# Kernel optimization log

Hardware: AMD Instinct MI355X
Metric: run time of the kernel (lower is better)

Reference implementation:

```python
import jax, jax.numpy as jnp
import numpy as np
import math


def _rope(x, cos, sin):
    # x: [B, S, h, hd]; cos/sin: [S, hd//2]
    B, S, h, hd = x.shape
    xr = x.reshape(B, S, h, hd // 2, 2)
    x_re, x_im = xr[..., 0], xr[..., 1]
    c = cos[None, :, None, :]
    s = sin[None, :, None, :]
    out_re = x_re * c - x_im * s
    out_im = x_re * s + x_im * c
    return jnp.stack([out_re, out_im], axis=-1).reshape(B, S, h, hd)


def setup_inputs() -> dict:
    key = jax.random.key(0)
    ks = jax.random.split(key, 8)
    B, S, D = 2, 2048, 2048
    H, G = 16, 4
    hd = D // H  # 128
    q = jax.random.normal(ks[0], (B, S, D), dtype=jnp.float32)
    k = jax.random.normal(ks[1], (B, S, D), dtype=jnp.float32)
    v = jax.random.normal(ks[2], (B, S, D), dtype=jnp.float32)
    # causal mask, matching typical usage (mask==0 -> -inf)
    mask = jnp.broadcast_to(jnp.tril(jnp.ones((S, S), dtype=jnp.int32)), (B, S, S))
    # RoPE freqs: thetas = base**(-2*arange(0,hd,2)/hd), freq = outer(m, thetas)
    exp = -2.0 * jnp.arange(0, hd, 2, dtype=jnp.float32) / hd
    thetas = jnp.power(10000.0, exp)
    m = jnp.arange(S, dtype=jnp.float32)
    freq = jnp.outer(m, thetas)  # [S, hd//2]
    freq_cos = jnp.cos(freq)
    freq_sin = jnp.sin(freq)
    sc = 0.02
    W_q = jax.random.normal(ks[3], (D, D), dtype=jnp.float32) * sc
    W_k = jax.random.normal(ks[4], (D, D // G), dtype=jnp.float32) * sc
    W_v = jax.random.normal(ks[5], (D, D // G), dtype=jnp.float32) * sc
    W_o = jax.random.normal(ks[6], (D, D), dtype=jnp.float32) * sc
    return {"q": q, "k": k, "v": v, "mask": mask, "freq_cos": freq_cos,
            "freq_sin": freq_sin, "W_q": W_q, "W_k": W_k, "W_v": W_v,
            "W_o": W_o, "heads": 16, "group_size": 4}


def reference(q, k, v, mask, freq_cos, freq_sin, W_q, W_k, W_v, W_o, heads, group_size):
    B, S, D = q.shape
    H = heads
    Hkv = H // group_size
    hd = D // H
    qp = (q @ W_q).reshape(B, S, H, hd)
    kp = (k @ W_k).reshape(B, S, Hkv, hd)
    vp = (v @ W_v).reshape(B, S, Hkv, hd)
    qp = _rope(qp, freq_cos, freq_sin)
    kp = _rope(kp, freq_cos, freq_sin)
    # repeat_kv: each kv head repeated group_size times (group index inner)
    kp = jnp.repeat(kp, group_size, axis=2)  # [B,S,H,hd]
    vp = jnp.repeat(vp, group_size, axis=2)
    qh = qp.transpose(0, 2, 1, 3)  # [B,H,S,hd]
    kh = kp.transpose(0, 2, 1, 3)
    vh = vp.transpose(0, 2, 1, 3)
    scores = jnp.einsum('bhqd,bhkd->bhqk', qh, kh) / math.sqrt(hd)
    scores = jnp.where(mask[:, None, :, :] == 0, jnp.float32(-1e9), scores)
    attn = jax.nn.softmax(scores, axis=-1)
    out = jnp.einsum('bhqk,bhkd->bhqd', attn, vh)  # [B,H,S,hd]
    out = out.transpose(0, 2, 1, 3).reshape(B, S, D)
    return out @ W_o
```

## Files before the change

kernel.cpp:

```cpp
#include <hip/hip_runtime.h>

typedef __bf16 bf16;
typedef __attribute__((ext_vector_type(8))) __bf16 bf16x8;
typedef __attribute__((ext_vector_type(4))) __bf16 bf16x4;
typedef __attribute__((ext_vector_type(4))) float f32x4;

#define MFMA16(a, b, c) __builtin_amdgcn_mfma_f32_16x16x32_bf16((a), (b), (c), 0, 0, 0)

typedef __attribute__((address_space(1))) const void* gas_t;
typedef __attribute__((address_space(3))) void* las_t;
#define GLOAD_LDS16(g, l) \
    __builtin_amdgcn_global_load_lds((gas_t)(g), (las_t)(l), 16, 0, 0)

__device__ __forceinline__ unsigned pack2(float a, float b) {
    unsigned short ua = __builtin_bit_cast(unsigned short, (bf16)a);
    unsigned short ub = __builtin_bit_cast(unsigned short, (bf16)b);
    return ((unsigned)ub << 16) | (unsigned)ua;
}

__global__ void transpose_cvt4(const float* __restrict__ Wq,
                               const float* __restrict__ Wo,
                               const float* __restrict__ Wk,
                               const float* __restrict__ Wv,
                               bf16* __restrict__ WqT, bf16* __restrict__ WoT,
                               bf16* __restrict__ WkT, bf16* __restrict__ WvT) {
    __shared__ bf16 tile[32][33];
    int z = blockIdx.z;
    const float* W = (z == 0) ? Wq : (z == 1) ? Wo : (z == 2) ? Wk : Wv;
    bf16* Wt = (z == 0) ? WqT : (z == 1) ? WoT : (z == 2) ? WkT : WvT;
    int N = (z < 2) ? 2048 : 512;
    const int K = 2048;
    int n0 = blockIdx.x * 32;
    if (n0 >= N) return;
    int k0 = blockIdx.y * 32;
    int tx = threadIdx.x, ty = threadIdx.y;
#pragma unroll
    for (int j = 0; j < 4; ++j)
        tile[ty + j * 8][tx] = (bf16)W[(size_t)(k0 + ty + j * 8) * N + n0 + tx];
    __syncthreads();
#pragma unroll
    for (int j = 0; j < 4; ++j)
        Wt[(size_t)(n0 + ty + j * 8) * K + k0 + tx] = tile[tx][ty + j * 8];
}

template <bool A_F32, bool DO_ROPE, int OUT_MODE>
__global__ __launch_bounds__(256) void gemm_bt(
    const void* __restrict__ Ain, const bf16* __restrict__ Bt,
    void* __restrict__ Cout, const float* __restrict__ cosb,
    const float* __restrict__ sinb, float scale, int Nn, int Kk) {
    __shared__ bf16 As[128 * 64];
    __shared__ bf16 Bs[128 * 64];
    int tid = threadIdx.x;
    int lane = tid & 63, wid = tid >> 6;
    int lr = lane & 15, lg = lane >> 4;
    int m0 = blockIdx.y * 128, n0 = blockIdx.x * 128;
    int wr = wid >> 1, wc = wid & 1;

    int srow = lane >> 3;
    int scol = ((lane & 7) ^ srow) << 3;
    const bf16* Bbase = Bt + (size_t)(n0 + wid * 32 + srow) * Kk + scol;
    const bf16* Abase_h =
        A_F32 ? nullptr
              : (const bf16*)Ain + (size_t)(m0 + wid * 32 + srow) * Kk + scol;

    int fragAr = wr * 64 + lr;
    int fragBr = wc * 64 + lr;
    int swz = lr & 7;

    f32x4 acc[4][4] = {};

    const int nk = Kk >> 6;
    for (int kt = 0; kt < nk; ++kt) {
        int k0 = kt << 6;
        if constexpr (A_F32) {
            const float* A = (const float*)Ain;
#pragma unroll
            for (int i = 0; i < 8; ++i) {
                int slot = tid + i * 256;
                int row = slot >> 4, c4 = (slot & 15) << 2;
                f32x4 v = *reinterpret_cast<const f32x4*>(
                    A + (size_t)(m0 + row) * Kk + k0 + c4);
                bf16x4 h;
                h[0] = (bf16)v[0]; h[1] = (bf16)v[1];
                h[2] = (bf16)v[2]; h[3] = (bf16)v[3];
                int blk = (c4 >> 3) ^ (row & 7);
                *reinterpret_cast<bf16x4*>(
                    &As[row * 64 + (blk << 3) + (c4 & 7)]) = h;
            }
        } else {
#pragma unroll
            for (int i = 0; i < 4; ++i)
                GLOAD_LDS16(Abase_h + (size_t)(i * 8) * Kk + k0,
                            &As[(wid * 4 + i) * 512]);
        }
#pragma unroll
        for (int i = 0; i < 4; ++i)
            GLOAD_LDS16(Bbase + (size_t)(i * 8) * Kk + k0,
                        &Bs[(wid * 4 + i) * 512]);
        __syncthreads();
#pragma unroll
        for (int kk = 0; kk < 2; ++kk) {
            int colOff = ((((kk << 2) | lg) ^ swz) << 3);
            bf16x8 af[4], bfr[4];
#pragma unroll
            for (int mi = 0; mi < 4; ++mi)
                af[mi] = *reinterpret_cast<const bf16x8*>(
                    &As[(fragAr + mi * 16) * 64 + colOff]);
#pragma unroll
            for (int ni = 0; ni < 4; ++ni)
                bfr[ni] = *reinterpret_cast<const bf16x8*>(
                    &Bs[(fragBr + ni * 16) * 64 + colOff]);
#pragma unroll
            for (int mi = 0; mi < 4; ++mi)
#pragma unroll
                for (int ni = 0; ni < 4; ++ni)
                    acc[mi][ni] = MFMA16(af[mi], bfr[ni], acc[mi][ni]);
        }
        __syncthreads();
    }

    int m_base = m0 + wr * 64, n_base = n0 + wc * 64;
#pragma unroll
    for (int mi = 0; mi < 4; ++mi) {
#pragma unroll
        for (int ni = 0; ni < 4; ++ni) {
            f32x4 v = acc[mi][ni];
            int gn = n_base + ni * 16 + lr;
            if constexpr (DO_ROPE) {
                int d = gn & 127, p = d >> 1;
                bool ev = ((d & 1) == 0);
#pragma unroll
                for (int r = 0; r < 4; ++r) {
                    int gm = m_base + mi * 16 + lg * 4 + r;
                    int s = gm & 2047;
                    float cc = cosb[s * 64 + p];
                    float ss = sinb[s * 64 + p];
                    float oth = __shfl_xor(v[r], 1);
                    v[r] = (ev ? (v[r] * cc - oth * ss)
                               : (oth * ss + v[r] * cc)) * scale;
                }
            }
            if constexpr (OUT_MODE == 0) {
                bf16* C = (bf16*)Cout;
#pragma unroll
                for (int r = 0; r < 4; ++r)
                    C[(size_t)(m_base + mi * 16 + lg * 4 + r) * Nn + gn] =
                        (bf16)v[r];
            } else {
                float* C = (float*)Cout;
#pragma unroll
                for (int r = 0; r < 4; ++r)
                    C[(size_t)(m_base + mi * 16 + lg * 4 + r) * Nn + gn] = v[r];
            }
        }
    }
}

__global__ __launch_bounds__(256) void gemm_kv(
    const float* __restrict__ kin, const float* __restrict__ vin,
    const bf16* __restrict__ WkT, const bf16* __restrict__ WvT,
    bf16* __restrict__ Kt, bf16* __restrict__ Vt,
    const float* __restrict__ cosb, const float* __restrict__ sinb) {
    const int Nn = 512, Kk = 2048;
    __shared__ bf16 As[128 * 64];
    __shared__ bf16 Bs[128 * 64];
    bool isK = (blockIdx.z == 0);
    const float* A = isK ? kin : vin;
    const bf16* Bt = isK ? WkT : WvT;

    int tid = threadIdx.x;
    int lane = tid & 63, wid = tid >> 6;
    int lr = lane & 15, lg = lane >> 4;
    int m0 = blockIdx.y * 128, n0 = blockIdx.x * 128;
    int wr = wid >> 1, wc = wid & 1;

    int srow = lane >> 3;
    int scol = ((lane & 7) ^ srow) << 3;
    const bf16* Bbase = Bt + (size_t)(n0 + wid * 32 + srow) * Kk + scol;

    int fragAr = wr * 64 + lr;
    int fragBr = wc * 64 + lr;
    int swz = lr & 7;

    f32x4 acc[4][4] = {};

    for (int kt = 0; kt < 32; ++kt) {
        int k0 = kt << 6;
#pragma unroll
        for (int i = 0; i < 8; ++i) {
            int slot = tid + i * 256;
            int row = slot >> 4, c4 = (slot & 15) << 2;
            f32x4 v = *reinterpret_cast<const f32x4*>(
                A + (size_t)(m0 + row) * Kk + k0 + c4);
            bf16x4 h;
            h[0] = (bf16)v[0]; h[1] = (bf16)v[1];
            h[2] = (bf16)v[2]; h[3] = (bf16)v[3];
            int blk = (c4 >> 3) ^ (row & 7);
            *reinterpret_cast<bf16x4*>(&As[row * 64 + (blk << 3) + (c4 & 7)]) = h;
        }
#pragma unroll
        for (int i = 0; i < 4; ++i)
            GLOAD_LDS16(Bbase + (size_t)(i * 8) * Kk + k0,
                        &Bs[(wid * 4 + i) * 512]);
        __syncthreads();
#pragma unroll
        for (int kk = 0; kk < 2; ++kk) {
            int colOff = ((((kk << 2) | lg) ^ swz) << 3);
            bf16x8 af[4], bfr[4];
#pragma unroll
            for (int mi = 0; mi < 4; ++mi)
                af[mi] = *reinterpret_cast<const bf16x8*>(
                    &As[(fragAr + mi * 16) * 64 + colOff]);
#pragma unroll
            for (int ni = 0; ni < 4; ++ni)
                bfr[ni] = *reinterpret_cast<const bf16x8*>(
                    &Bs[(fragBr + ni * 16) * 64 + colOff]);
#pragma unroll
            for (int mi = 0; mi < 4; ++mi)
#pragma unroll
                for (int ni = 0; ni < 4; ++ni)
                    acc[mi][ni] = MFMA16(af[mi], bfr[ni], acc[mi][ni]);
        }
        __syncthreads();
    }

    int m_base = m0 + wr * 64, n_base = n0 + wc * 64;
#pragma unroll
    for (int mi = 0; mi < 4; ++mi) {
#pragma unroll
        for (int ni = 0; ni < 4; ++ni) {
            f32x4 v = acc[mi][ni];
            int gn = n_base + ni * 16 + lr;
            int hkv = gn >> 7, d = gn & 127;
            if (isK) {
                int p = d >> 1;
                bool ev = ((d & 1) == 0);
#pragma unroll
                for (int r = 0; r < 4; ++r) {
                    int gm = m_base + mi * 16 + lg * 4 + r;
                    int s = gm & 2047;
                    float cc = cosb[s * 64 + p];
                    float ss = sinb[s * 64 + p];
                    float oth = __shfl_xor(v[r], 1);
                    float rv = ev ? (v[r] * cc - oth * ss) : (oth * ss + v[r] * cc);
                    int bb = gm >> 11;
                    Kt[((size_t)(bb * 4 + hkv) * 2048 + s) * 128 + d] = (bf16)rv;
                }
            } else {
                int gm0 = m_base + mi * 16 + lg * 4;
                int bb = gm0 >> 11, s = gm0 & 2047;
                bf16x4 hh;
#pragma unroll
                for (int r = 0; r < 4; ++r) hh[r] = (bf16)v[r];
                *reinterpret_cast<bf16x4*>(
                    Vt + ((size_t)(bb * 4 + hkv) * 128 + d) * 2048 + s) = hh;
            }
        }
    }
}

__global__ __launch_bounds__(256) void attn_kernel(
    const bf16* __restrict__ Qp, const bf16* __restrict__ Kt,
    const bf16* __restrict__ Vt, bf16* __restrict__ Ao) {
    const int S = 2048, H = 16, HKV = 4, HD = 128;
    __shared__ bf16 Klds[64][136];
    __shared__ bf16 Vlds[128][72];

    int tid = threadIdx.x, lane = tid & 63, wid = tid >> 6;
    int lr = lane & 15, lg = lane >> 4;
    int h = blockIdx.x, b = blockIdx.y;
    int qt = (int)(gridDim.z - 1) - (int)blockIdx.z;
    int hkv = h >> 2;
    int q0 = qt * 64 + wid * 16;
    int qrow = q0 + lr;

    const bf16* Kbase = Kt + (size_t)(b * HKV + hkv) * S * HD;
    const bf16* Vbase = Vt + (size_t)(b * HKV + hkv) * HD * S;

    bf16x8 qf[4];
    {
        const bf16* qb = Qp + ((size_t)(b * S + qrow) * H + h) * HD;
#pragma unroll
        for (int ks = 0; ks < 4; ++ks)
            qf[ks] = *reinterpret_cast<const bf16x8*>(qb + ks * 32 + lg * 8);
    }

    f32x4 O[8] = {};
    float m_run = -3e38f, l_run = 0.f;
    int src0 = ((lane >> 4) & 1) * 32 + lr;
    int src1 = src0 + 16;
    bool h1 = (lg >> 1) != 0;

    for (int kb = 0; kb <= qt; ++kb) {
        int s0 = kb * 64;
        bf16x8 kreg[4], vreg[4];
#pragma unroll
        for (int i = 0; i < 4; ++i) {
            int slot = tid + i * 256;
            int krow = slot >> 4, kc = (slot & 15) << 3;
            kreg[i] = *reinterpret_cast<const bf16x8*>(
                Kbase + (size_t)(s0 + krow) * HD + kc);
            int vrow = slot >> 3, vc = (slot & 7) << 3;
            vreg[i] = *reinterpret_cast<const bf16x8*>(
                Vbase + (size_t)vrow * S + s0 + vc);
        }
#pragma unroll
        for (int i = 0; i < 4; ++i) {
            int slot = tid + i * 256;
            int krow = slot >> 4, kc = (slot & 15) << 3;
            *reinterpret_cast<bf16x8*>(&Klds[krow][kc]) = kreg[i];
            int vrow = slot >> 3, vc = (slot & 7) << 3;
            *reinterpret_cast<bf16x8*>(&Vlds[vrow][vc]) = vreg[i];
        }
        __syncthreads();

        float p[4][4];
#pragma unroll
        for (int nt = 0; nt < 4; ++nt) {
            f32x4 sc = {};
#pragma unroll
            for (int ks = 0; ks < 4; ++ks) {
                bf16x8 kf = *reinterpret_cast<const bf16x8*>(
                    &Klds[nt * 16 + lr][ks * 32 + lg * 8]);
                sc = MFMA16(kf, qf[ks], sc);
            }
            if (kb == qt) {
                int sa = s0 + nt * 16 + lg * 4;
#pragma unroll
                for (int r = 0; r < 4; ++r)
                    p[nt][r] = (sa + r <= qrow) ? sc[r] : -1e30f;
            } else {
#pragma unroll
                for (int r = 0; r < 4; ++r) p[nt][r] = sc[r];
            }
        }
        float mx = p[0][0];
#pragma unroll
        for (int nt = 0; nt < 4; ++nt)
#pragma unroll
            for (int r = 0; r < 4; ++r) mx = fmaxf(mx, p[nt][r]);
        mx = fmaxf(mx, __shfl_xor(mx, 16));
        mx = fmaxf(mx, __shfl_xor(mx, 32));
        float mnew = fmaxf(m_run, mx);
        float al = __expf(m_run - mnew);
        m_run = mnew;
        float rs = 0.f;
#pragma unroll
        for (int nt = 0; nt < 4; ++nt)
#pragma unroll
            for (int r = 0; r < 4; ++r) {
                p[nt][r] = __expf(p[nt][r] - mnew);
                rs += p[nt][r];
            }
        rs += __shfl_xor(rs, 16);
        rs += __shfl_xor(rs, 32);
        l_run = l_run * al + rs;

        unsigned pk00 = pack2(p[0][0], p[0][1]), pk01 = pack2(p[0][2], p[0][3]);
        unsigned pk10 = pack2(p[1][0], p[1][1]), pk11 = pack2(p[1][2], p[1][3]);
        unsigned pk20 = pack2(p[2][0], p[2][1]), pk21 = pack2(p[2][2], p[2][3]);
        unsigned pk30 = pack2(p[3][0], p[3][1]), pk31 = pack2(p[3][2], p[3][3]);
        unsigned e00 = __shfl(pk00, src0), e01 = __shfl(pk01, src0);
        unsigned e10 = __shfl(pk10, src0), e11 = __shfl(pk11, src0);
        unsigned e20 = __shfl(pk20, src0), e21 = __shfl(pk21, src0);
        unsigned e30 = __shfl(pk30, src0), e31 = __shfl(pk31, src0);
        unsigned o00 = __shfl(pk00, src1), o01 = __shfl(pk01, src1);
        unsigned o10 = __shfl(pk10, src1), o11 = __shfl(pk11, src1);
        unsigned o20 = __shfl(pk20, src1), o21 = __shfl(pk21, src1);
        unsigned o30 = __shfl(pk30, src1), o31 = __shfl(pk31, src1);
        union U { unsigned u[4]; bf16x8 v; } P0, P1;
        P0.u[0] = h1 ? e10 : e00;
        P0.u[1] = h1 ? e11 : e01;
        P0.u[2] = h1 ? o10 : o00;
        P0.u[3] = h1 ? o11 : o01;
        P1.u[0] = h1 ? e30 : e20;
        P1.u[1] = h1 ? e31 : e21;
        P1.u[2] = h1 ? o30 : o20;
        P1.u[3] = h1 ? o31 : o21;

#pragma unroll
        for (int d2 = 0; d2 < 8; ++d2)
#pragma unroll
            for (int r = 0; r < 4; ++r) O[d2][r] *= al;
#pragma unroll
        for (int d2 = 0; d2 < 8; ++d2) {
            bf16x8 vf0 =
                *reinterpret_cast<const bf16x8*>(&Vlds[d2 * 16 + lr][lg * 8]);
            bf16x8 vf1 = *reinterpret_cast<const bf16x8*>(
                &Vlds[d2 * 16 + lr][32 + lg * 8]);
            O[d2] = MFMA16(vf0, P0.v, O[d2]);
            O[d2] = MFMA16(vf1, P1.v, O[d2]);
        }
        __syncthreads();
    }

    float inv = 1.0f / l_run;
    const size_t obase = ((size_t)(b * S + qrow) * H + h) * HD;
#pragma unroll
    for (int d2 = 0; d2 < 8; ++d2) {
        bf16x4 st;
#pragma unroll
        for (int r = 0; r < 4; ++r) st[r] = (bf16)(O[d2][r] * inv);
        *reinterpret_cast<bf16x4*>(const_cast<bf16*>(Ao) + obase + d2 * 16 +
                                   lg * 4) = st;
    }
}

extern "C" void kernel_launch(void* const* d_in, const int* in_sizes, int n_in,
                              void* d_out, int out_size, void* d_ws,
                              size_t ws_size, hipStream_t stream) {
    const float* q = (const float*)d_in[0];
    const float* k = (const float*)d_in[1];
    const float* v = (const float*)d_in[2];
    const float* fc = (const float*)d_in[4];
    const float* fs = (const float*)d_in[5];
    const float* Wq = (const float*)d_in[6];
    const float* Wk = (const float*)d_in[7];
    const float* Wv = (const float*)d_in[8];
    const float* Wo = (const float*)d_in[9];

    char* ws = (char*)d_ws;
    bf16* Wq_t = (bf16*)(ws + 0);
    bf16* Wk_t = (bf16*)(ws + 8388608);
    bf16* Wv_t = (bf16*)(ws + 10485760);
    bf16* Wo_t = (bf16*)(ws + 12582912);
    bf16* Qp   = (bf16*)(ws + 20971520);
    bf16* Kt   = (bf16*)(ws + 37748736);
    bf16* Vt   = (bf16*)(ws + 41943040);
    bf16* Ao   = (bf16*)(ws + 46137344);

    transpose_cvt4<<<dim3(64, 64, 4), dim3(32, 8), 0, stream>>>(
        Wq, Wo, Wk, Wv, Wq_t, Wo_t, Wk_t, Wv_t);

    const float qscale = 0.08838834764831845f;

    gemm_bt<true, true, 0><<<dim3(16, 32), 256, 0, stream>>>(
        (const void*)q, Wq_t, (void*)Qp, fc, fs, qscale, 2048, 2048);
    gemm_kv<<<dim3(4, 32, 2), 256, 0, stream>>>(k, v, Wk_t, Wv_t, Kt, Vt, fc,
                                                fs);

    attn_kernel<<<dim3(16, 2, 32), 256, 0, stream>>>(Qp, Kt, Vt, Ao);

    gemm_bt<false, false, 1><<<dim3(16, 32), 256, 0, stream>>>(
        (const void*)Ao, Wo_t, d_out, fc, fs, 1.0f, 2048, 2048);
}
```

Measured before the change: 277.0 us.

## Prefetch next K/V tile in attention and fold log2e into Q scale

The attention loop now issues the global loads for the next K/V block into registers right after the LDS barrier, so they overlap the QK, softmax and PV math of the current block instead of sitting at the start of each iteration. The Q scale is premultiplied by log2(e) so softmax can call exp2f instead of __expf. The templated gemm_bt is split into specialised gemm_q and gemm_o kernels, which mainly removes template branches. The prefetch costs extra registers, which may lower occupancy.

Result: faster. 270.4 us (-2.4%).

```diff
diff --git a/kernel.cpp b/kernel.cpp
--- a/kernel.cpp
+++ b/kernel.cpp
@@ -43,11 +43,11 @@
         Wt[(size_t)(n0 + ty + j * 8) * K + k0 + tx] = tile[tx][ty + j * 8];
 }
 
-template <bool A_F32, bool DO_ROPE, int OUT_MODE>
-__global__ __launch_bounds__(256) void gemm_bt(
-    const void* __restrict__ Ain, const bf16* __restrict__ Bt,
-    void* __restrict__ Cout, const float* __restrict__ cosb,
-    const float* __restrict__ sinb, float scale, int Nn, int Kk) {
+__global__ __launch_bounds__(256) void gemm_q(
+    const float* __restrict__ A, const bf16* __restrict__ Bt,
+    bf16* __restrict__ Qp, const float* __restrict__ cosb,
+    const float* __restrict__ sinb, float qscale) {
+    const int Kk = 2048, Nn = 2048;
     __shared__ bf16 As[128 * 64];
     __shared__ bf16 Bs[128 * 64];
     int tid = threadIdx.x;
@@ -59,9 +59,6 @@
     int srow = lane >> 3;
     int scol = ((lane & 7) ^ srow) << 3;
     const bf16* Bbase = Bt + (size_t)(n0 + wid * 32 + srow) * Kk + scol;
-    const bf16* Abase_h =
-        A_F32 ? nullptr
-              : (const bf16*)Ain + (size_t)(m0 + wid * 32 + srow) * Kk + scol;
 
     int fragAr = wr * 64 + lr;
     int fragBr = wc * 64 + lr;
@@ -69,29 +66,19 @@
 
     f32x4 acc[4][4] = {};
 
-    const int nk = Kk >> 6;
-    for (int kt = 0; kt < nk; ++kt) {
+    for (int kt = 0; kt < 32; ++kt) {
         int k0 = kt << 6;
-        if constexpr (A_F32) {
-            const float* A = (const float*)Ain;
-#pragma unroll
-            for (int i = 0; i < 8; ++i) {
-                int slot = tid + i * 256;
-                int row = slot >> 4, c4 = (slot & 15) << 2;
-                f32x4 v = *reinterpret_cast<const f32x4*>(
-                    A + (size_t)(m0 + row) * Kk + k0 + c4);
-                bf16x4 h;
-                h[0] = (bf16)v[0]; h[1] = (bf16)v[1];
-                h[2] = (bf16)v[2]; h[3] = (bf16)v[3];
-                int blk = (c4 >> 3) ^ (row & 7);
-                *reinterpret_cast<bf16x4*>(
-                    &As[row * 64 + (blk << 3) + (c4 & 7)]) = h;
-            }
-        } else {
-#pragma unroll
-            for (int i = 0; i < 4; ++i)
-                GLOAD_LDS16(Abase_h + (size_t)(i * 8) * Kk + k0,
-                            &As[(wid * 4 + i) * 512]);
+#pragma unroll
+        for (int i = 0; i < 8; ++i) {
+            int slot = tid + i * 256;
+            int row = slot >> 4, c4 = (slot & 15) << 2;
+            f32x4 v = *reinterpret_cast<const f32x4*>(
+                A + (size_t)(m0 + row) * Kk + k0 + c4);
+            bf16x4 h;
+            h[0] = (bf16)v[0]; h[1] = (bf16)v[1];
+            h[2] = (bf16)v[2]; h[3] = (bf16)v[3];
+            int blk = (c4 >> 3) ^ (row & 7);
+            *reinterpret_cast<bf16x4*>(&As[row * 64 + (blk << 3) + (c4 & 7)]) = h;
         }
 #pragma unroll
         for (int i = 0; i < 4; ++i)
@@ -126,32 +113,22 @@
         for (int ni = 0; ni < 4; ++ni) {
             f32x4 v = acc[mi][ni];
             int gn = n_base + ni * 16 + lr;
-            if constexpr (DO_ROPE) {
-                int d = gn & 127, p = d >> 1;
-                bool ev = ((d & 1) == 0);
-#pragma unroll
-                for (int r = 0; r < 4; ++r) {
-                    int gm = m_base + mi * 16 + lg * 4 + r;
-                    int s = gm & 2047;
-                    float cc = cosb[s * 64 + p];
-                    float ss = sinb[s * 64 + p];
-                    float oth = __shfl_xor(v[r], 1);
-                    v[r] = (ev ? (v[r] * cc - oth * ss)
-                               : (oth * ss + v[r] * cc)) * scale;
-                }
+            int d = gn & 127, p = d >> 1;
+            bool ev = ((d & 1) == 0);
+#pragma unroll
+            for (int r = 0; r < 4; ++r) {
+                int gm = m_base + mi * 16 + lg * 4 + r;
+                int s = gm & 2047;
+                float cc = cosb[s * 64 + p];
+                float ss = sinb[s * 64 + p];
+                float oth = __shfl_xor(v[r], 1);
+                v[r] = (ev ? (v[r] * cc - oth * ss)
+                           : (oth * ss + v[r] * cc)) * qscale;
             }
-            if constexpr (OUT_MODE == 0) {
-                bf16* C = (bf16*)Cout;
-#pragma unroll
-                for (int r = 0; r < 4; ++r)
-                    C[(size_t)(m_base + mi * 16 + lg * 4 + r) * Nn + gn] =
-                        (bf16)v[r];
-            } else {
-                float* C = (float*)Cout;
-#pragma unroll
-                for (int r = 0; r < 4; ++r)
-                    C[(size_t)(m_base + mi * 16 + lg * 4 + r) * Nn + gn] = v[r];
-            }
+#pragma unroll
+            for (int r = 0; r < 4; ++r)
+                Qp[(size_t)(m_base + mi * 16 + lg * 4 + r) * Nn + gn] =
+                    (bf16)v[r];
         }
     }
 }
@@ -161,7 +138,7 @@
     const bf16* __restrict__ WkT, const bf16* __restrict__ WvT,
     bf16* __restrict__ Kt, bf16* __restrict__ Vt,
     const float* __restrict__ cosb, const float* __restrict__ sinb) {
-    const int Nn = 512, Kk = 2048;
+    const int Kk = 2048;
     __shared__ bf16 As[128 * 64];
     __shared__ bf16 Bs[128 * 64];
     bool isK = (blockIdx.z == 0);
@@ -259,6 +236,73 @@
     }
 }
 
+__global__ __launch_bounds__(256) void gemm_o(
+    const bf16* __restrict__ Ain, const bf16* __restrict__ Bt,
+    float* __restrict__ Cout, int Nn, int Kk) {
+    __shared__ bf16 As[128 * 64];
+    __shared__ bf16 Bs[128 * 64];
+    int tid = threadIdx.x;
+    int lane = tid & 63, wid = tid >> 6;
+    int lr = lane & 15, lg = lane >> 4;
+    int m0 = blockIdx.y * 128, n0 = blockIdx.x * 128;
+    int wr = wid >> 1, wc = wid & 1;
+
+    int srow = lane >> 3;
+    int scol = ((lane & 7) ^ srow) << 3;
+    const bf16* Bbase = Bt + (size_t)(n0 + wid * 32 + srow) * Kk + scol;
+    const bf16* Abase = Ain + (size_t)(m0 + wid * 32 + srow) * Kk + scol;
+
+    int fragAr = wr * 64 + lr;
+    int fragBr = wc * 64 + lr;
+    int swz = lr & 7;
+
+    f32x4 acc[4][4] = {};
+
+    const int nk = Kk >> 6;
+    for (int kt = 0; kt < nk; ++kt) {
+        int k0 = kt << 6;
+#pragma unroll
+        for (int i = 0; i < 4; ++i) {
+            GLOAD_LDS16(Abase + (size_t)(i * 8) * Kk + k0,
+                        &As[(wid * 4 + i) * 512]);
+            GLOAD_LDS16(Bbase + (size_t)(i * 8) * Kk + k0,
+                        &Bs[(wid * 4 + i) * 512]);
+        }
+        __syncthreads();
+#pragma unroll
+        for (int kk = 0; kk < 2; ++kk) {
+            int colOff = ((((kk << 2) | lg) ^ swz) << 3);
+            bf16x8 af[4], bfr[4];
+#pragma unroll
+            for (int mi = 0; mi < 4; ++mi)
+                af[mi] = *reinterpret_cast<const bf16x8*>(
+                    &As[(fragAr + mi * 16) * 64 + colOff]);
+#pragma unroll
+            for (int ni = 0; ni < 4; ++ni)
+                bfr[ni] = *reinterpret_cast<const bf16x8*>(
+                    &Bs[(fragBr + ni * 16) * 64 + colOff]);
+#pragma unroll
+            for (int mi = 0; mi < 4; ++mi)
+#pragma unroll
+                for (int ni = 0; ni < 4; ++ni)
+                    acc[mi][ni] = MFMA16(af[mi], bfr[ni], acc[mi][ni]);
+        }
+        __syncthreads();
+    }
+
+    int m_base = m0 + wr * 64, n_base = n0 + wc * 64;
+#pragma unroll
+    for (int mi = 0; mi < 4; ++mi)
+#pragma unroll
+        for (int ni = 0; ni < 4; ++ni) {
+            f32x4 v = acc[mi][ni];
+            int gn = n_base + ni * 16 + lr;
+#pragma unroll
+            for (int r = 0; r < 4; ++r)
+                Cout[(size_t)(m_base + mi * 16 + lg * 4 + r) * Nn + gn] = v[r];
+        }
+}
+
 __global__ __launch_bounds__(256) void attn_kernel(
     const bf16* __restrict__ Qp, const bf16* __restrict__ Kt,
     const bf16* __restrict__ Vt, bf16* __restrict__ Ao) {
@@ -291,28 +335,41 @@
     int src1 = src0 + 16;
     bool h1 = (lg >> 1) != 0;
 
-    for (int kb = 0; kb <= qt; ++kb) {
+    int nkb = qt + 1;
+    int k_r[4], k_c[4], v_r[4], v_c[4];
+#pragma unroll
+    for (int i = 0; i < 4; ++i) {
+        int slot = tid + i * 256;
+        k_r[i] = slot >> 4; k_c[i] = (slot & 15) << 3;
+        v_r[i] = slot >> 3; v_c[i] = (slot & 7) << 3;
+    }
+    bf16x8 kreg[4], vreg[4];
+#pragma unroll
+    for (int i = 0; i < 4; ++i) {
+        kreg[i] = *reinterpret_cast<const bf16x8*>(
+            Kbase + (size_t)k_r[i] * HD + k_c[i]);
+        vreg[i] = *reinterpret_cast<const bf16x8*>(
+            Vbase + (size_t)v_r[i] * S + v_c[i]);
+    }
+
+    for (int kb = 0; kb < nkb; ++kb) {
         int s0 = kb * 64;
-        bf16x8 kreg[4], vreg[4];
 #pragma unroll
         for (int i = 0; i < 4; ++i) {
-            int slot = tid + i * 256;
-            int krow = slot >> 4, kc = (slot & 15) << 3;
-            kreg[i] = *reinterpret_cast<const bf16x8*>(
-                Kbase + (size_t)(s0 + krow) * HD + kc);
-            int vrow = slot >> 3, vc = (slot & 7) << 3;
-            vreg[i] = *reinterpret_cast<const bf16x8*>(
-                Vbase + (size_t)vrow * S + s0 + vc);
-        }
-#pragma unroll
-        for (int i = 0; i < 4; ++i) {
-            int slot = tid + i * 256;
-            int krow = slot >> 4, kc = (slot & 15) << 3;
-            *reinterpret_cast<bf16x8*>(&Klds[krow][kc]) = kreg[i];
-            int vrow = slot >> 3, vc = (slot & 7) << 3;
-            *reinterpret_cast<bf16x8*>(&Vlds[vrow][vc]) = vreg[i];
-        }
-        __syncthreads();
+            *reinterpret_cast<bf16x8*>(&Klds[k_r[i]][k_c[i]]) = kreg[i];
+            *reinterpret_cast<bf16x8*>(&Vlds[v_r[i]][v_c[i]]) = vreg[i];
+        }
+        __syncthreads();
+        if (kb + 1 < nkb) {
+            int sn = s0 + 64;
+#pragma unroll
+            for (int i = 0; i < 4; ++i) {
+                kreg[i] = *reinterpret_cast<const bf16x8*>(
+                    Kbase + (size_t)(sn + k_r[i]) * HD + k_c[i]);
+                vreg[i] = *reinterpret_cast<const bf16x8*>(
+                    Vbase + (size_t)v_r[i] * S + sn + v_c[i]);
+            }
+        }
 
         float p[4][4];
 #pragma unroll
@@ -342,14 +399,14 @@
         mx = fmaxf(mx, __shfl_xor(mx, 16));
         mx = fmaxf(mx, __shfl_xor(mx, 32));
         float mnew = fmaxf(m_run, mx);
-        float al = __expf(m_run - mnew);
+        float al = exp2f(m_run - mnew);
         m_run = mnew;
         float rs = 0.f;
 #pragma unroll
         for (int nt = 0; nt < 4; ++nt)
 #pragma unroll
             for (int r = 0; r < 4; ++r) {
-                p[nt][r] = __expf(p[nt][r] - mnew);
+                p[nt][r] = exp2f(p[nt][r] - mnew);
                 rs += p[nt][r];
             }
         rs += __shfl_xor(rs, 16);
@@ -432,15 +489,14 @@
     transpose_cvt4<<<dim3(64, 64, 4), dim3(32, 8), 0, stream>>>(
         Wq, Wo, Wk, Wv, Wq_t, Wo_t, Wk_t, Wv_t);
 
-    const float qscale = 0.08838834764831845f;
-
-    gemm_bt<true, true, 0><<<dim3(16, 32), 256, 0, stream>>>(
-        (const void*)q, Wq_t, (void*)Qp, fc, fs, qscale, 2048, 2048);
+    const float qscale = 0.08838834764831845f * 1.4426950408889634f;
+
+    gemm_q<<<dim3(16, 32), 256, 0, stream>>>(q, Wq_t, Qp, fc, fs, qscale);
     gemm_kv<<<dim3(4, 32, 2), 256, 0, stream>>>(k, v, Wk_t, Wv_t, Kt, Vt, fc,
                                                 fs);
 
     attn_kernel<<<dim3(16, 2, 32), 256, 0, stream>>>(Qp, Kt, Vt, Ao);
 
-    gemm_bt<false, false, 1><<<dim3(16, 32), 256, 0, stream>>>(
-        (const void*)Ao, Wo_t, d_out, fc, fs, 1.0f, 2048, 2048);
-}
+    gemm_o<<<dim3(16, 32), 256, 0, stream>>>(Ao, Wo_t, (float*)d_out, 2048,
+                                             2048);
+}
```
